# Kernel optimization log

Measured on AMD Instinct MI355X. Metric: run time of the kernel, lower is better.

Reference implementation:

```python
import jax, jax.numpy as jnp
import numpy as np

N_NODES = 100000
N_EDGES = 1600000
IN_DIM = 128
HID = 256
N_GRAPHS = 256
N_OUT = 2


def setup_inputs() -> dict:
    key = jax.random.key(0)
    ks = jax.random.split(key, 16)
    s_in = 1.0 / np.sqrt(IN_DIM)
    s_h = 1.0 / np.sqrt(HID)
    return {
        "x": jax.random.normal(ks[0], (N_NODES, IN_DIM), jnp.float32),
        "W_pool": jax.random.normal(ks[1], (IN_DIM, IN_DIM), jnp.float32) * s_in,
        "b_pool": jnp.zeros((IN_DIM,), jnp.float32),
        "W_self": jax.random.normal(ks[2], (IN_DIM, HID), jnp.float32) * s_in,
        "W_neigh": jax.random.normal(ks[3], (IN_DIM, HID), jnp.float32) * s_in,
        "b_sage": jnp.zeros((HID,), jnp.float32),
        "W1": jax.random.normal(ks[4], (HID, HID), jnp.float32) * s_h,
        "b1": jnp.zeros((HID,), jnp.float32),
        "W2": jax.random.normal(ks[5], (HID, HID), jnp.float32) * s_h,
        "b2": jnp.zeros((HID,), jnp.float32),
        "Wr": jax.random.normal(ks[6], (HID, N_OUT), jnp.float32) * s_h,
        "br": jnp.zeros((N_OUT,), jnp.float32),
        "src": jax.random.randint(ks[7], (N_EDGES,), 0, N_NODES, jnp.int32),
        "dst": jax.random.randint(ks[8], (N_EDGES,), 0, N_NODES, jnp.int32),
        "graph_id": jnp.sort(jax.random.randint(ks[9], (N_NODES,), 0, N_GRAPHS, jnp.int32)),
    }


def reference(x, W_pool, b_pool, W_self, W_neigh, b_sage, W1, b1, W2, b2, Wr, br, src, dst, graph_id):
    n = x.shape[0]
    # --- SAGEConv 'pool' aggregator ---
    m = jax.nn.relu(x @ W_pool + b_pool)                      # [N, IN]
    neigh = jax.ops.segment_max(m[src], dst, num_segments=n)  # max over in-neighbors
    neigh = jnp.where(jnp.isfinite(neigh), neigh, 0.0)        # isolated nodes -> 0 (DGL zero-init)
    h = jax.nn.relu(x @ W_self + neigh @ W_neigh + b_sage)    # [N, HID]
    # --- MLP stack ---
    h = jax.nn.relu(h @ W1 + b1)
    h = jax.nn.relu(h @ W2 + b2)
    # --- softmax_nodes: per-graph softmax over nodes, per feature ---
    gmax = jax.ops.segment_max(h, graph_id, num_segments=N_GRAPHS)
    gmax = jnp.where(jnp.isfinite(gmax), gmax, 0.0)
    z = jnp.exp(h - gmax[graph_id])                           # [N, HID]
    zsum = jax.ops.segment_sum(z, graph_id, num_segments=N_GRAPHS)
    hg = z / zsum[graph_id]
    # --- max_nodes readout ---
    final = jax.ops.segment_max(hg, graph_id, num_segments=N_GRAPHS)
    final = jnp.where(jnp.isfinite(final), final, 0.0)        # [G, HID]
    return final @ Wr + br                                    # [G, N_OUT]
```

## Files before the change

### kernel.cpp

```cpp
#include <hip/hip_runtime.h>

#define N_NODES  100000
#define N_EDGES  1600000
#define IN_DIM   128
#define HID      256
#define N_GRAPHS 256
#define ESHIFT   20.0f
#define BSH      7
#define NB2      782

typedef _Float16 f16x8 __attribute__((ext_vector_type(8)));
typedef float f32x16 __attribute__((ext_vector_type(16)));
#define MFMA16(a, b, c) __builtin_amdgcn_mfma_f32_32x32x16_f16((a), (b), (c), 0, 0, 0)

#define PKMAX(a, b) asm("v_pk_max_f16 %0, %0, %1" : "+v"(a) : "v"(b))

static __device__ __forceinline__ unsigned short f2h_bits(float f) {
    _Float16 h = (_Float16)f;
    return __builtin_bit_cast(unsigned short, h);
}
static __device__ __forceinline__ float h2f(unsigned short b) {
    return (float)__builtin_bit_cast(_Float16, b);
}

static __device__ __forceinline__ void decode_blk(int M, int& m0, int& n0)
{
    const int gmb = (M + 127) >> 7;
    const int l = blockIdx.x;
    int mb, nb;
    if ((int)gridDim.x == gmb) {
        mb = l; nb = 0;
    } else {
        const int nfull = (gmb >> 3) << 4;
        if (l < nfull) {
            mb = ((l >> 4) << 3) | (l & 7);
            nb = (l >> 3) & 1;
        } else {
            const int t = l - nfull, tm = gmb & 7;
            mb = (gmb & ~7) + (t % tm);
            nb = t / tm;
        }
    }
    m0 = mb * 128;
    n0 = nb * 128;
}

__global__ __launch_bounds__(256) void x_to_h(
    const float* __restrict__ in, unsigned short* __restrict__ xh, int n)
{
    int i = (blockIdx.x * 256 + threadIdx.x) * 4;
    if (i < n) {
        float4 v = *(const float4*)&in[i];
        ushort4 h;
        h.x = f2h_bits(v.x); h.y = f2h_bits(v.y);
        h.z = f2h_bits(v.z); h.w = f2h_bits(v.w);
        *(ushort4*)&xh[i] = h;
    }
}

__global__ __launch_bounds__(256) void w_split_h(
    const float* __restrict__ Wa, const float* __restrict__ Wb, int K1,
    int K, int N, unsigned short* __restrict__ hi, unsigned short* __restrict__ lo)
{
    int idx = blockIdx.x * 256 + threadIdx.x;
    if (idx >= K * N) return;
    int k = idx / N, n = idx - k * N;
    float w = (k < K1) ? Wa[(size_t)k * N + n] : Wb[(size_t)(k - K1) * N + n];
    unsigned short h = f2h_bits(w);
    unsigned short l = f2h_bits(w - h2f(h));
    hi[(size_t)n * K + k] = h;
    lo[(size_t)n * K + k] = l;
}

__global__ __launch_bounds__(256) void gemm_mfma_h(
    const unsigned short* __restrict__ A1, const unsigned short* __restrict__ A2,
    int K1, int Ktot,
    const unsigned short* __restrict__ Wh, const unsigned short* __restrict__ Wl,
    const float* __restrict__ bias, void* __restrict__ Cv,
    int M, int N, int mode)
{
    __shared__ __align__(16) short tA [128][32];
    __shared__ __align__(16) short tBh[128][32];
    __shared__ __align__(16) short tBl[128][32];

    const int tid  = threadIdx.x;
    int m0, n0;
    decode_blk(M, m0, n0);
    const int wave = tid >> 6, lane = tid & 63;
    const int mw   = (wave & 1) * 64, nw = (wave >> 1) * 64;
    const int lm   = lane & 31;

    const int rsub = lane >> 2;
    const int kqe  = ((lane & 3) ^ ((lane >> 3) & 3)) << 3;
    const int rw   = wave << 5;

    const int s4  = (lm >> 1) & 3;
    const int cB  = lane >> 5;
    const int ch0 = ((cB ^ s4) << 3);
    const int ch1 = (((2 | cB) ^ s4) << 3);
    const f16x8* a00 = (const f16x8*)&tA [mw + lm     ][ch0];
    const f16x8* a01 = (const f16x8*)&tA [mw + lm     ][ch1];
    const f16x8* a10 = (const f16x8*)&tA [mw + 32 + lm][ch0];
    const f16x8* a11 = (const f16x8*)&tA [mw + 32 + lm][ch1];
    const f16x8* bh00 = (const f16x8*)&tBh[nw + lm     ][ch0];
    const f16x8* bh01 = (const f16x8*)&tBh[nw + lm     ][ch1];
    const f16x8* bh10 = (const f16x8*)&tBh[nw + 32 + lm][ch0];
    const f16x8* bh11 = (const f16x8*)&tBh[nw + 32 + lm][ch1];
    const f16x8* bl00 = (const f16x8*)&tBl[nw + lm     ][ch0];
    const f16x8* bl01 = (const f16x8*)&tBl[nw + lm     ][ch1];
    const f16x8* bl10 = (const f16x8*)&tBl[nw + 32 + lm][ch0];
    const f16x8* bl11 = (const f16x8*)&tBl[nw + 32 + lm][ch1];

    f32x16 acc[4];
#pragma unroll
    for (int t = 0; t < 4; ++t)
#pragma unroll
        for (int i = 0; i < 16; ++i) acc[t][i] = 0.f;

    for (int kc = 0; kc < Ktot; kc += 32) {
        const unsigned short* Ab; int Astr, kl;
        if (kc < K1) { Ab = A1; Astr = K1;        kl = kc; }
        else         { Ab = A2; Astr = Ktot - K1; kl = kc - K1; }

        __syncthreads();
#pragma unroll
        for (int j = 0; j < 2; ++j) {
            const int tr = rw + j * 16;
            int row = m0 + tr + rsub; if (row >= M) row = M - 1;
            __builtin_amdgcn_global_load_lds(
                Ab + (size_t)row * Astr + kl + kqe, &tA[tr][0], 16, 0, 0);
            const size_t o = (size_t)(n0 + tr + rsub) * Ktot + kc + kqe;
            __builtin_amdgcn_global_load_lds(Wh + o, &tBh[tr][0], 16, 0, 0);
            __builtin_amdgcn_global_load_lds(Wl + o, &tBl[tr][0], 16, 0, 0);
        }
        __syncthreads();

        {
            f16x8 A0 = *a00, A1f = *a10;
            f16x8 B0h = *bh00, B1h = *bh10, B0l = *bl00, B1l = *bl10;
            acc[0] = MFMA16(A0,  B0h, acc[0]);
            acc[1] = MFMA16(A0,  B1h, acc[1]);
            acc[2] = MFMA16(A1f, B0h, acc[2]);
            acc[3] = MFMA16(A1f, B1h, acc[3]);
            acc[0] = MFMA16(A0,  B0l, acc[0]);
            acc[1] = MFMA16(A0,  B1l, acc[1]);
            acc[2] = MFMA16(A1f, B0l, acc[2]);
            acc[3] = MFMA16(A1f, B1l, acc[3]);
        }
        {
            f16x8 A0 = *a01, A1f = *a11;
            f16x8 B0h = *bh01, B1h = *bh11, B0l = *bl01, B1l = *bl11;
            acc[0] = MFMA16(A0,  B0h, acc[0]);
            acc[1] = MFMA16(A0,  B1h, acc[1]);
            acc[2] = MFMA16(A1f, B0h, acc[2]);
            acc[3] = MFMA16(A1f, B1h, acc[3]);
            acc[0] = MFMA16(A0,  B0l, acc[0]);
            acc[1] = MFMA16(A0,  B1l, acc[1]);
            acc[2] = MFMA16(A1f, B0l, acc[2]);
            acc[3] = MFMA16(A1f, B1l, acc[3]);
        }
    }

    const int rb = 4 * (lane >> 5);
#pragma unroll
    for (int ti = 0; ti < 2; ++ti)
#pragma unroll
    for (int tj = 0; tj < 2; ++tj) {
        f32x16 a = acc[ti * 2 + tj];
        int coln = n0 + nw + tj * 32 + lm;
        float bv = bias[coln];
#pragma unroll
        for (int reg = 0; reg < 16; ++reg) {
            int rrow = m0 + mw + ti * 32 + (reg & 3) + 8 * (reg >> 2) + rb;
            if (rrow < M) {
                float v = a[reg] + bv;
                v = v > 0.f ? v : 0.f;
                size_t o = (size_t)rrow * N + coln;
                if (mode == 0) ((float*)Cv)[o] = v;
                else           ((unsigned short*)Cv)[o] = f2h_bits(v);
            }
        }
    }
}

__global__ __launch_bounds__(256) void gemm_fused_sm(
    const unsigned short* __restrict__ A1,
    int Ktot,
    const unsigned short* __restrict__ Wh, const unsigned short* __restrict__ Wl,
    const float* __restrict__ bias, const int* __restrict__ gid,
    float* __restrict__ pm, float* __restrict__ ps,
    int M, int N)
{
    __shared__ __align__(16) short tA [128][32];
    __shared__ __align__(16) short tBh[128][32];
    __shared__ __align__(16) short tBl[128][32];

    const int tid  = threadIdx.x;
    int m0, n0;
    decode_blk(M, m0, n0);
    const int wave = tid >> 6, lane = tid & 63;
    const int mw   = (wave & 1) * 64, nw = (wave >> 1) * 64;
    const int lm   = lane & 31;

    const int rsub = lane >> 2;
    const int kqe  = ((lane & 3) ^ ((lane >> 3) & 3)) << 3;
    const int rw   = wave << 5;

    const int s4  = (lm >> 1) & 3;
    const int cB  = lane >> 5;
    const int ch0 = ((cB ^ s4) << 3);
    const int ch1 = (((2 | cB) ^ s4) << 3);
    const f16x8* a00 = (const f16x8*)&tA [mw + lm     ][ch0];
    const f16x8* a01 = (const f16x8*)&tA [mw + lm     ][ch1];
    const f16x8* a10 = (const f16x8*)&tA [mw + 32 + lm][ch0];
    const f16x8* a11 = (const f16x8*)&tA [mw + 32 + lm][ch1];
    const f16x8* bh00 = (const f16x8*)&tBh[nw + lm     ][ch0];
    const f16x8* bh01 = (const f16x8*)&tBh[nw + lm     ][ch1];
    const f16x8* bh10 = (const f16x8*)&tBh[nw + 32 + lm][ch0];
    const f16x8* bh11 = (const f16x8*)&tBh[nw + 32 + lm][ch1];
    const f16x8* bl00 = (const f16x8*)&tBl[nw + lm     ][ch0];
    const f16x8* bl01 = (const f16x8*)&tBl[nw + lm     ][ch1];
    const f16x8* bl10 = (const f16x8*)&tBl[nw + 32 + lm][ch0];
    const f16x8* bl11 = (const f16x8*)&tBl[nw + 32 + lm][ch1];

    f32x16 acc[4];
#pragma unroll
    for (int t = 0; t < 4; ++t)
#pragma unroll
        for (int i = 0; i < 16; ++i) acc[t][i] = 0.f;

    for (int kc = 0; kc < Ktot; kc += 32) {
        __syncthreads();
#pragma unroll
        for (int j = 0; j < 2; ++j) {
            const int tr = rw + j * 16;
            int row = m0 + tr + rsub; if (row >= M) row = M - 1;
            __builtin_amdgcn_global_load_lds(
                A1 + (size_t)row * Ktot + kc + kqe, &tA[tr][0], 16, 0, 0);
            const size_t o = (size_t)(n0 + tr + rsub) * Ktot + kc + kqe;
            __builtin_amdgcn_global_load_lds(Wh + o, &tBh[tr][0], 16, 0, 0);
            __builtin_amdgcn_global_load_lds(Wl + o, &tBl[tr][0], 16, 0, 0);
        }
        __syncthreads();

        {
            f16x8 A0 = *a00, A1f = *a10;
            f16x8 B0h = *bh00, B1h = *bh10, B0l = *bl00, B1l = *bl10;
            acc[0] = MFMA16(A0,  B0h, acc[0]);
            acc[1] = MFMA16(A0,  B1h, acc[1]);
            acc[2] = MFMA16(A1f, B0h, acc[2]);
            acc[3] = MFMA16(A1f, B1h, acc[3]);
            acc[0] = MFMA16(A0,  B0l, acc[0]);
            acc[1] = MFMA16(A0,  B1l, acc[1]);
            acc[2] = MFMA16(A1f, B0l, acc[2]);
            acc[3] = MFMA16(A1f, B1l, acc[3]);
        }
        {
            f16x8 A0 = *a01, A1f = *a11;
            f16x8 B0h = *bh01, B1h = *bh11, B0l = *bl01, B1l = *bl11;
            acc[0] = MFMA16(A0,  B0h, acc[0]);
            acc[1] = MFMA16(A0,  B1h, acc[1]);
            acc[2] = MFMA16(A1f, B0h, acc[2]);
            acc[3] = MFMA16(A1f, B1h, acc[3]);
            acc[0] = MFMA16(A0,  B0l, acc[0]);
            acc[1] = MFMA16(A0,  B1l, acc[1]);
            acc[2] = MFMA16(A1f, B0l, acc[2]);
            acc[3] = MFMA16(A1f, B1l, acc[3]);
        }
    }

    __syncthreads();
    float* sS = (float*)&tA[0][0];
    int*   sM = (int*)&tBh[0][0];
    for (int i = tid; i < 512; i += 256) { sS[i] = 0.f; sM[i] = 0; }
    __syncthreads();

    const int gfirst = gid[m0];
    const int rlast  = (m0 + 127 < M) ? (m0 + 127) : (M - 1);
    const int span   = gid[rlast] - gfirst + 1;

    const int rb = 4 * (lane >> 5);
#pragma unroll
    for (int tj = 0; tj < 2; ++tj) {
        int coln = n0 + nw + tj * 32 + lm;
        int cl   = coln - n0;
        float bv = bias[coln];
        int run_g = -1; float run_s = 0.f, run_m = 0.f;
#pragma unroll
        for (int ti = 0; ti < 2; ++ti) {
            f32x16 a = acc[ti * 2 + tj];
#pragma unroll
            for (int reg = 0; reg < 16; ++reg) {
                int rrow = m0 + mw + ti * 32 + (reg & 3) + 8 * (reg >> 2) + rb;
                if (rrow >= M) continue;
                float v = a[reg] + bv;
                v = v > 0.f ? v : 0.f;
                int g = gid[rrow];
                if (g != run_g) {
                    if (run_g >= 0) {
                        int slot = run_g - gfirst;
                        if (slot < 4) {
                            atomicAdd(&sS[slot * 128 + cl], run_s);
                            atomicMax(&sM[slot * 128 + cl], __float_as_int(run_m));
                        } else {
                            atomicAdd(&ps[(size_t)run_g * HID + coln], run_s);
                            atomicMax((int*)&pm[(size_t)run_g * HID + coln],
                                      __float_as_int(run_m));
                        }
                    }
                    run_g = g; run_s = 0.f; run_m = 0.f;
                }
                run_s += __expf(v - ESHIFT);
                run_m = fmaxf(run_m, v);
            }
        }
        if (run_g >= 0) {
            int slot = run_g - gfirst;
            if (slot < 4) {
                atomicAdd(&sS[slot * 128 + cl], run_s);
                atomicMax(&sM[slot * 128 + cl], __float_as_int(run_m));
            } else {
                atomicAdd(&ps[(size_t)run_g * HID + coln], run_s);
                atomicMax((int*)&pm[(size_t)run_g * HID + coln],
                          __float_as_int(run_m));
            }
        }
    }
    __syncthreads();

    int lim = (span < 4 ? span : 4) * 128;
    for (int i = tid; i < lim; i += 256) {
        int s = i >> 7, c = i & 127;
        float vs = sS[i];
        if (vs > 0.f) {
            int g = gfirst + s;
            atomicAdd(&ps[(size_t)g * HID + n0 + c], vs);
            atomicMax((int*)&pm[(size_t)g * HID + n0 + c], sM[i]);
        }
    }
}

__global__ __launch_bounds__(256) void part_count(
    const int* __restrict__ dst, int* __restrict__ btot, int E)
{
    __shared__ int sh[NB2];
    const int t = threadIdx.x;
    for (int i = t; i < NB2; i += 256) sh[i] = 0;
    __syncthreads();
    int base = blockIdx.x * 4096 + t;
#pragma unroll
    for (int i = 0; i < 16; ++i) {
        int e = base + i * 256;
        if (e < E) atomicAdd(&sh[dst[e] >> BSH], 1);
    }
    __syncthreads();
    for (int i = t; i < NB2; i += 256)
        if (sh[i]) atomicAdd(&btot[i], sh[i]);
}

__global__ __launch_bounds__(256) void scan_b(
    const int* __restrict__ btot, int* __restrict__ bstart,
    int* __restrict__ cursor, int total)
{
    __shared__ int sh[256];
    const int t = threadIdx.x;
    int a[4];
    int s = 0;
#pragma unroll
    for (int i = 0; i < 4; ++i) {
        int idx = t * 4 + i;
        a[i] = (idx < NB2) ? btot[idx] : 0;
        s += a[i];
    }
    sh[t] = s;
    __syncthreads();
    for (int off = 1; off < 256; off <<= 1) {
        int v = (t >= off) ? sh[t - off] : 0;
        __syncthreads();
        if (t >= off) sh[t] += v;
        __syncthreads();
    }
    int run = (t > 0) ? sh[t - 1] : 0;
#pragma unroll
    for (int i = 0; i < 4; ++i) {
        int idx = t * 4 + i;
        if (idx < NB2) { bstart[idx] = run; cursor[idx] = run; }
        run += a[i];
    }
    if (t == 0) bstart[NB2] = total;
}

__global__ __launch_bounds__(256) void part_scatter(
    const int* __restrict__ src, const int* __restrict__ dst,
    int* __restrict__ cursor, int2* __restrict__ pairs, int E)
{
    __shared__ int cnt[NB2], goff[NB2], fill[NB2];
    const int t = threadIdx.x;
    const int base = blockIdx.x * 4096;
    for (int i = t; i < NB2; i += 256) { cnt[i] = 0; fill[i] = 0; }
    __syncthreads();
    int myd[16];
#pragma unroll
    for (int i = 0; i < 16; ++i) {
        int e = base + t + i * 256;
        myd[i] = (e < E) ? dst[e] : -1;
        if (myd[i] >= 0) atomicAdd(&cnt[myd[i] >> BSH], 1);
    }
    __syncthreads();
    for (int i = t; i < NB2; i += 256)
        goff[i] = cnt[i] ? atomicAdd(&cursor[i], cnt[i]) : 0;
    __syncthreads();
#pragma unroll
    for (int i = 0; i < 16; ++i) {
        int e = base + t + i * 256;
        if (myd[i] >= 0) {
            int b = myd[i] >> BSH;
            int r = atomicAdd(&fill[b], 1);
            pairs[goff[b] + r] = make_int2(myd[i], src[e]);
        }
    }
}

__global__ __launch_bounds__(256) void bucket_sort(
    const int2* __restrict__ pairs, const int* __restrict__ bstart,
    int* __restrict__ csr_src, int* __restrict__ offs, int Nn, int E)
{
    __shared__ int cnt[128], off[128];
    const int b = blockIdx.x;
    const int t = threadIdx.x;
    const int lo = bstart[b], hi = bstart[b + 1];
    if (t < 128) cnt[t] = 0;
    __syncthreads();
    for (int e = lo + t; e < hi; e += 256)
        atomicAdd(&cnt[pairs[e].x & 127], 1);
    __syncthreads();
    if (t == 0) {
        int s = 0;
        for (int i = 0; i < 128; ++i) { off[i] = s; s += cnt[i]; }
    }
    __syncthreads();
    if (t < 128) {
        int node = (b << BSH) + t;
        if (node < Nn) offs[node] = lo + off[t];
        cnt[t] = off[t];
    }
    if (b == NB2 - 1 && t == 0) offs[Nn] = E;
    __syncthreads();
    for (int e = lo + t; e < hi; e += 256) {
        int2 p = pairs[e];
        int r = atomicAdd(&cnt[p.x & 127], 1);
        csr_src[lo + r] = p.y;
    }
}

__global__ __launch_bounds__(256) void csr_max_agg_h(
    const unsigned short* __restrict__ m, const int* __restrict__ csr_src,
    const int* __restrict__ offs, unsigned short* __restrict__ neigh, int Nn)
{
    const int node = (blockIdx.x * 256 + threadIdx.x) >> 6;
    const int lane = threadIdx.x & 63;
    if (node >= Nn) return;
    const int e0  = offs[node];
    const int end = offs[node + 1];
    const char* mc = (const char*)m;

    uint4 acc = make_uint4(0u, 0u, 0u, 0u);
    if (end > e0) {
        const unsigned fo = (unsigned)(lane & 15) << 4;
        const int sub = lane >> 4;
        for (int base = e0; base < end; base += 64) {
            int ee = base + lane;
            int sl = csr_src[ee < end ? ee : (end - 1)];
            int cnt = end - base; if (cnt > 64) cnt = 64;
            int iters = (cnt + 3) >> 2;
            for (int j = 0; j < iters; ++j) {
                int s = __shfl(sl, (j << 2) | sub);
                uint4 v = *(const uint4*)(mc + (((unsigned)s << 8) | fo));
                PKMAX(acc.x, v.x);
                PKMAX(acc.y, v.y);
                PKMAX(acc.z, v.z);
                PKMAX(acc.w, v.w);
            }
        }
        uint4 o;
        o.x = __shfl_xor(acc.x, 16); o.y = __shfl_xor(acc.y, 16);
        o.z = __shfl_xor(acc.z, 16); o.w = __shfl_xor(acc.w, 16);
        PKMAX(acc.x, o.x); PKMAX(acc.y, o.y);
        PKMAX(acc.z, o.z); PKMAX(acc.w, o.w);
        o.x = __shfl_xor(acc.x, 32); o.y = __shfl_xor(acc.y, 32);
        o.z = __shfl_xor(acc.z, 32); o.w = __shfl_xor(acc.w, 32);
        PKMAX(acc.x, o.x); PKMAX(acc.y, o.y);
        PKMAX(acc.z, o.z); PKMAX(acc.w, o.w);
    }
    if (lane < 16)
        *(uint4*)((char*)neigh + (((size_t)node << 8) | ((unsigned)lane << 4))) = acc;
}

__global__ __launch_bounds__(256) void softmax_merge(
    const float* __restrict__ pm, const float* __restrict__ ps,
    const float* __restrict__ Wr, const float* __restrict__ brv,
    float* __restrict__ out)
{
    const int g = blockIdx.x;
    const int j = threadIdx.x;

    float M = pm[(size_t)g * HID + j];
    float S = ps[(size_t)g * HID + j];
    float fm = (S > 0.f) ? __expf(M - ESHIFT) / S : 0.f;

    float p0 = fm * Wr[j * 2 + 0];
    float p1 = fm * Wr[j * 2 + 1];
#pragma unroll
    for (int off = 32; off > 0; off >>= 1) {
        p0 += __shfl_down(p0, off);
        p1 += __shfl_down(p1, off);
    }
    __shared__ float red[8];
    int wv = j >> 6, ln = j & 63;
    if (ln == 0) { red[wv * 2] = p0; red[wv * 2 + 1] = p1; }
    __syncthreads();
    if (j == 0) out[g * 2 + 0] = red[0] + red[2] + red[4] + red[6] + brv[0];
    if (j == 1) out[g * 2 + 1] = red[1] + red[3] + red[5] + red[7] + brv[1];
}

extern "C" void kernel_launch(void* const* d_in, const int* in_sizes, int n_in,
                              void* d_out, int out_size, void* d_ws, size_t ws_size,
                              hipStream_t stream)
{
    const float* x      = (const float*)d_in[0];
    const float* W_pool = (const float*)d_in[1];
    const float* b_pool = (const float*)d_in[2];
    const float* W_self = (const float*)d_in[3];
    const float* W_neigh= (const float*)d_in[4];
    const float* b_sage = (const float*)d_in[5];
    const float* W1     = (const float*)d_in[6];
    const float* b1     = (const float*)d_in[7];
    const float* W2     = (const float*)d_in[8];
    const float* b2     = (const float*)d_in[9];
    const float* Wr     = (const float*)d_in[10];
    const float* br     = (const float*)d_in[11];
    const int*   src    = (const int*)d_in[12];
    const int*   dst    = (const int*)d_in[13];
    const int*   gid    = (const int*)d_in[14];

    const int Nn = N_NODES, E = N_EDGES;
    char* ws = (char*)d_ws;

    unsigned short* xh    = (unsigned short*)(ws + 0);
    unsigned short* m_buf = (unsigned short*)(ws + 25600000);
    unsigned short* neigh = (unsigned short*)(ws + 51200000);
    int2*           pairs = (int2*)(ws + 76800000);
    int*            btot  = (int*)(ws + 89600000);
    int*            bstart= btot + NB2;
    int*            cursor= bstart + NB2 + 1;
    float*          pm    = (float*)(ws + 90000000);
    float*          ps    = pm + (size_t)N_GRAPHS * HID;
    int*            offs  = (int*)(ws + 91000000);
    int*            csr_src = (int*)(ws + 91500000);
    unsigned short* h1    = (unsigned short*)(ws + 102400000);
    unsigned short* h2    = (unsigned short*)(ws + 153600000);

    char* srcws = (char*)(void*)src;
    unsigned short* wpool_h = (unsigned short*)(srcws + 0);
    unsigned short* wpool_l = wpool_h + 128 * 128;
    unsigned short* wsage_h = wpool_l + 128 * 128;
    unsigned short* wsage_l = wsage_h + 256 * 256;
    unsigned short* w1_h    = wsage_l + 256 * 256;
    unsigned short* w1_l    = w1_h + 256 * 256;
    unsigned short* w2_h    = w1_l + 256 * 256;
    unsigned short* w2_l    = w2_h + 256 * 256;

    dim3 blk(256);
    const int gm = (Nn + 127) / 128;
    const int pchunks = (E + 4095) / 4096;

    hipMemsetAsync(btot, 0, NB2 * sizeof(int), stream);
    hipMemsetAsync(pm, 0, (size_t)2 * N_GRAPHS * HID * sizeof(float), stream);

    x_to_h<<<dim3((Nn * IN_DIM / 4 + 255) / 256), blk, 0, stream>>>(
        x, xh, Nn * IN_DIM);

    part_count<<<dim3(pchunks), blk, 0, stream>>>(dst, btot, E);
    scan_b<<<dim3(1), blk, 0, stream>>>(btot, bstart, cursor, E);
    part_scatter<<<dim3(pchunks), blk, 0, stream>>>(src, dst, cursor, pairs, E);
    bucket_sort<<<dim3(NB2), blk, 0, stream>>>(pairs, bstart, csr_src, offs, Nn, E);

    w_split_h<<<dim3((128 * 128 + 255) / 256), blk, 0, stream>>>(
        W_pool, W_pool, 128, 128, 128, wpool_h, wpool_l);
    w_split_h<<<dim3((256 * 256 + 255) / 256), blk, 0, stream>>>(
        W_self, W_neigh, 128, 256, 256, wsage_h, wsage_l);
    w_split_h<<<dim3((256 * 256 + 255) / 256), blk, 0, stream>>>(
        W1, W1, 256, 256, 256, w1_h, w1_l);
    w_split_h<<<dim3((256 * 256 + 255) / 256), blk, 0, stream>>>(
        W2, W2, 256, 256, 256, w2_h, w2_l);

    gemm_mfma_h<<<dim3(gm), blk, 0, stream>>>(
        xh, xh, 128, 128, wpool_h, wpool_l, b_pool, m_buf, Nn, 128, 1);

    csr_max_agg_h<<<dim3((Nn * 64 + 255) / 256), blk, 0, stream>>>(
        m_buf, csr_src, offs, neigh, Nn);

    gemm_mfma_h<<<dim3(2 * gm), blk, 0, stream>>>(
        xh, neigh, 128, 256, wsage_h, wsage_l, b_sage, h1, Nn, 256, 1);

    gemm_mfma_h<<<dim3(2 * gm), blk, 0, stream>>>(
        h1, h1, 256, 256, w1_h, w1_l, b1, h2, Nn, 256, 1);

    gemm_fused_sm<<<dim3(2 * gm), blk, 0, stream>>>(
        h2, 256, w2_h, w2_l, b2, gid, pm, ps, Nn, 256);

    softmax_merge<<<dim3(N_GRAPHS), blk, 0, stream>>>(pm, ps, Wr, br, (float*)d_out);
}
```

Measured before the change: 471.1 us.

## Use persistent GEMMs with register-resident weights and double-buffered A tiles

Replaces the three 256-wide GEMMs with persistent 512-thread kernels on a 256-block grid. Each wave keeps its 32 output columns of the split-fp16 weights in registers, and 64-row A tiles stream through a double-buffered LDS pipeline controlled by manual vmcnt waits. This removes the repeated weight tile loads and per-K-step block barriers of the old tiled kernel. The softmax-stat epilogue now keeps a running per-graph accumulator across a block's whole contiguous row range, with 8 shared slots. The costs are very high register pressure, which may limit occupancy, and a fixed grid size that can leave some blocks with an extra tile.

Result: faster. 434.5 us (-7.8%).

```diff
diff --git a/kernel.cpp b/kernel.cpp
--- a/kernel.cpp
+++ b/kernel.cpp
@@ -14,6 +14,9 @@
 #define MFMA16(a, b, c) __builtin_amdgcn_mfma_f32_32x32x16_f16((a), (b), (c), 0, 0, 0)
 
 #define PKMAX(a, b) asm("v_pk_max_f16 %0, %0, %1" : "+v"(a) : "v"(b))
+
+#define BARX() __builtin_amdgcn_s_barrier()
+#define WAITVM(N) asm volatile("s_waitcnt vmcnt(" #N ")" ::: "memory")
 
 static __device__ __forceinline__ unsigned short f2h_bits(float f) {
     _Float16 h = (_Float16)f;
@@ -183,115 +186,170 @@
     }
 }
 
-__global__ __launch_bounds__(256) void gemm_fused_sm(
-    const unsigned short* __restrict__ A1,
-    int Ktot,
+static __device__ __forceinline__ void stage_tile64(
+    const unsigned short* __restrict__ A1, const unsigned short* __restrict__ A2,
+    int K1, int M, int r0g, short* bufb, int wave, int lane)
+{
+    const int l5 = lane >> 5;
+    const int s  = lane & 31;
+#pragma unroll
+    for (int i = 0; i < 4; ++i) {
+        const int p    = wave * 4 + i;
+        const int rloc = 2 * p + l5;
+        int row = r0g + rloc; if (row >= M) row = M - 1;
+        const int c8 = ((s ^ ((2 * i + l5) & 7)) << 3);
+        const unsigned short* sp = (c8 < K1)
+            ? A1 + (size_t)row * K1 + c8
+            : A2 + (size_t)row * (256 - K1) + (c8 - K1);
+        __builtin_amdgcn_global_load_lds(sp, bufb + p * 512, 16, 0, 0);
+    }
+}
+
+__global__ __launch_bounds__(512, 2) void gemm_bstat(
+    const unsigned short* __restrict__ A1, const unsigned short* __restrict__ A2,
+    int K1,
+    const unsigned short* __restrict__ Wh, const unsigned short* __restrict__ Wl,
+    const float* __restrict__ bias, unsigned short* __restrict__ C,
+    unsigned short* __restrict__ dummy, int M)
+{
+    __shared__ __align__(16) short buf[2][64][256];
+
+    const int tid = threadIdx.x, wave = tid >> 6, lane = tid & 63;
+    const int lm = lane & 31, hib = lane >> 5;
+    const int col = wave * 32 + lm;
+    const int hi8 = hib * 8;
+
+    f16x8 Bh[16], Bl[16];
+#pragma unroll
+    for (int k = 0; k < 16; ++k) {
+        const size_t o = (size_t)col * 256 + k * 16 + hi8;
+        Bh[k] = *(const f16x8*)(Wh + o);
+        Bl[k] = *(const f16x8*)(Wl + o);
+    }
+
+    const int nt = (M + 63) >> 6;
+    const int G = gridDim.x, b = blockIdx.x;
+    const int q = nt / G, r = nt % G;
+    const int t0  = b * q + (b < r ? b : r);
+    const int ntl = q + (b < r ? 1 : 0);
+
+    const int rq    = (lm >> 1) & 3;
+    const int abase = lm * 512 + ((hib ^ (lm & 1)) << 4);
+    const float bv  = bias[col];
+    const int rb    = 4 * hib;
+
+    stage_tile64(A1, A2, K1, M, t0 << 6, &buf[0][0][0], wave, lane);
+    if (ntl > 1)
+        stage_tile64(A1, A2, K1, M, (t0 + 1) << 6, &buf[1][0][0], wave, lane);
+
+    for (int t = 0; t < ntl; ++t) {
+        if (t == 0) { if (ntl > 1) WAITVM(4); else WAITVM(0); }
+        else if (t + 1 < ntl) WAITVM(36);
+        else WAITVM(32);
+        BARX();
+
+        f32x16 acc0, acc1;
+#pragma unroll
+        for (int i = 0; i < 16; ++i) { acc0[i] = 0.f; acc1[i] = 0.f; }
+        const char* lb = (const char*)&buf[t & 1][0][0];
+#pragma unroll
+        for (int k = 0; k < 16; ++k) {
+            const int koff = ((k ^ rq) << 5);
+            f16x8 a0 = *(const f16x8*)(lb + abase + koff);
+            f16x8 a1 = *(const f16x8*)(lb + abase + koff + 16384);
+            acc0 = MFMA16(a0, Bh[k], acc0);
+            acc1 = MFMA16(a1, Bh[k], acc1);
+            acc0 = MFMA16(a0, Bl[k], acc0);
+            acc1 = MFMA16(a1, Bl[k], acc1);
+        }
+        BARX();
+
+        const int r0g = (t0 + t) << 6;
+#pragma unroll
+        for (int reg = 0; reg < 16; ++reg) {
+            const int rr0 = r0g + (reg & 3) + 8 * (reg >> 2) + rb;
+            const int rr1 = rr0 + 32;
+            unsigned short* d0 = (rr0 < M) ? C + (size_t)rr0 * 256 + col : dummy + tid;
+            unsigned short* d1 = (rr1 < M) ? C + (size_t)rr1 * 256 + col : dummy + tid;
+            *d0 = f2h_bits(fmaxf(acc0[reg] + bv, 0.f));
+            *d1 = f2h_bits(fmaxf(acc1[reg] + bv, 0.f));
+        }
+        if (t + 2 < ntl)
+            stage_tile64(A1, A2, K1, M, (t0 + t + 2) << 6,
+                         &buf[t & 1][0][0], wave, lane);
+    }
+}
+
+__global__ __launch_bounds__(512, 2) void gemm_bstat_sm(
+    const unsigned short* __restrict__ A,
     const unsigned short* __restrict__ Wh, const unsigned short* __restrict__ Wl,
     const float* __restrict__ bias, const int* __restrict__ gid,
-    float* __restrict__ pm, float* __restrict__ ps,
-    int M, int N)
-{
-    __shared__ __align__(16) short tA [128][32];
-    __shared__ __align__(16) short tBh[128][32];
-    __shared__ __align__(16) short tBl[128][32];
-
-    const int tid  = threadIdx.x;
-    int m0, n0;
-    decode_blk(M, m0, n0);
-    const int wave = tid >> 6, lane = tid & 63;
-    const int mw   = (wave & 1) * 64, nw = (wave >> 1) * 64;
-    const int lm   = lane & 31;
-
-    const int rsub = lane >> 2;
-    const int kqe  = ((lane & 3) ^ ((lane >> 3) & 3)) << 3;
-    const int rw   = wave << 5;
-
-    const int s4  = (lm >> 1) & 3;
-    const int cB  = lane >> 5;
-    const int ch0 = ((cB ^ s4) << 3);
-    const int ch1 = (((2 | cB) ^ s4) << 3);
-    const f16x8* a00 = (const f16x8*)&tA [mw + lm     ][ch0];
-    const f16x8* a01 = (const f16x8*)&tA [mw + lm     ][ch1];
-    const f16x8* a10 = (const f16x8*)&tA [mw + 32 + lm][ch0];
-    const f16x8* a11 = (const f16x8*)&tA [mw + 32 + lm][ch1];
-    const f16x8* bh00 = (const f16x8*)&tBh[nw + lm     ][ch0];
-    const f16x8* bh01 = (const f16x8*)&tBh[nw + lm     ][ch1];
-    const f16x8* bh10 = (const f16x8*)&tBh[nw + 32 + lm][ch0];
-    const f16x8* bh11 = (const f16x8*)&tBh[nw + 32 + lm][ch1];
-    const f16x8* bl00 = (const f16x8*)&tBl[nw + lm     ][ch0];
-    const f16x8* bl01 = (const f16x8*)&tBl[nw + lm     ][ch1];
-    const f16x8* bl10 = (const f16x8*)&tBl[nw + 32 + lm][ch0];
-    const f16x8* bl11 = (const f16x8*)&tBl[nw + 32 + lm][ch1];
-
-    f32x16 acc[4];
-#pragma unroll
-    for (int t = 0; t < 4; ++t)
-#pragma unroll
-        for (int i = 0; i < 16; ++i) acc[t][i] = 0.f;
-
-    for (int kc = 0; kc < Ktot; kc += 32) {
-        __syncthreads();
-#pragma unroll
-        for (int j = 0; j < 2; ++j) {
-            const int tr = rw + j * 16;
-            int row = m0 + tr + rsub; if (row >= M) row = M - 1;
-            __builtin_amdgcn_global_load_lds(
-                A1 + (size_t)row * Ktot + kc + kqe, &tA[tr][0], 16, 0, 0);
-            const size_t o = (size_t)(n0 + tr + rsub) * Ktot + kc + kqe;
-            __builtin_amdgcn_global_load_lds(Wh + o, &tBh[tr][0], 16, 0, 0);
-            __builtin_amdgcn_global_load_lds(Wl + o, &tBl[tr][0], 16, 0, 0);
-        }
-        __syncthreads();
-
-        {
-            f16x8 A0 = *a00, A1f = *a10;
-            f16x8 B0h = *bh00, B1h = *bh10, B0l = *bl00, B1l = *bl10;
-            acc[0] = MFMA16(A0,  B0h, acc[0]);
-            acc[1] = MFMA16(A0,  B1h, acc[1]);
-            acc[2] = MFMA16(A1f, B0h, acc[2]);
-            acc[3] = MFMA16(A1f, B1h, acc[3]);
-            acc[0] = MFMA16(A0,  B0l, acc[0]);
-            acc[1] = MFMA16(A0,  B1l, acc[1]);
-            acc[2] = MFMA16(A1f, B0l, acc[2]);
-            acc[3] = MFMA16(A1f, B1l, acc[3]);
-        }
-        {
-            f16x8 A0 = *a01, A1f = *a11;
-            f16x8 B0h = *bh01, B1h = *bh11, B0l = *bl01, B1l = *bl11;
-            acc[0] = MFMA16(A0,  B0h, acc[0]);
-            acc[1] = MFMA16(A0,  B1h, acc[1]);
-            acc[2] = MFMA16(A1f, B0h, acc[2]);
-            acc[3] = MFMA16(A1f, B1h, acc[3]);
-            acc[0] = MFMA16(A0,  B0l, acc[0]);
-            acc[1] = MFMA16(A0,  B1l, acc[1]);
-            acc[2] = MFMA16(A1f, B0l, acc[2]);
-            acc[3] = MFMA16(A1f, B1l, acc[3]);
-        }
-    }
-
-    __syncthreads();
-    float* sS = (float*)&tA[0][0];
-    int*   sM = (int*)&tBh[0][0];
-    for (int i = tid; i < 512; i += 256) { sS[i] = 0.f; sM[i] = 0; }
-    __syncthreads();
-
-    const int gfirst = gid[m0];
-    const int rlast  = (m0 + 127 < M) ? (m0 + 127) : (M - 1);
-    const int span   = gid[rlast] - gfirst + 1;
-
-    const int rb = 4 * (lane >> 5);
-#pragma unroll
-    for (int tj = 0; tj < 2; ++tj) {
-        int coln = n0 + nw + tj * 32 + lm;
-        int cl   = coln - n0;
-        float bv = bias[coln];
-        int run_g = -1; float run_s = 0.f, run_m = 0.f;
-#pragma unroll
-        for (int ti = 0; ti < 2; ++ti) {
-            f32x16 a = acc[ti * 2 + tj];
+    float* __restrict__ pm, float* __restrict__ ps, int M)
+{
+    __shared__ __align__(16) short buf[2][64][256];
+    __shared__ float sS[8 * 256];
+    __shared__ int   sM[8 * 256];
+
+    const int tid = threadIdx.x, wave = tid >> 6, lane = tid & 63;
+    const int lm = lane & 31, hib = lane >> 5;
+    const int col = wave * 32 + lm;
+    const int hi8 = hib * 8;
+
+    for (int i = tid; i < 2048; i += 512) { sS[i] = 0.f; sM[i] = 0; }
+
+    f16x8 Bh[16], Bl[16];
+#pragma unroll
+    for (int k = 0; k < 16; ++k) {
+        const size_t o = (size_t)col * 256 + k * 16 + hi8;
+        Bh[k] = *(const f16x8*)(Wh + o);
+        Bl[k] = *(const f16x8*)(Wl + o);
+    }
+
+    const int nt = (M + 63) >> 6;
+    const int G = gridDim.x, b = blockIdx.x;
+    const int q = nt / G, r = nt % G;
+    const int t0  = b * q + (b < r ? b : r);
+    const int ntl = q + (b < r ? 1 : 0);
+
+    const int rq    = (lm >> 1) & 3;
+    const int abase = lm * 512 + ((hib ^ (lm & 1)) << 4);
+    const float bv  = bias[col];
+    const int rb    = 4 * hib;
+    const int gfirst = gid[t0 << 6];
+
+    stage_tile64(A, A, 256, M, t0 << 6, &buf[0][0][0], wave, lane);
+    if (ntl > 1)
+        stage_tile64(A, A, 256, M, (t0 + 1) << 6, &buf[1][0][0], wave, lane);
+
+    int run_g = -1; float run_s = 0.f, run_m = 0.f;
+
+    for (int t = 0; t < ntl; ++t) {
+        if (t + 1 < ntl) WAITVM(4); else WAITVM(0);
+        BARX();
+
+        f32x16 acc0, acc1;
+#pragma unroll
+        for (int i = 0; i < 16; ++i) { acc0[i] = 0.f; acc1[i] = 0.f; }
+        const char* lb = (const char*)&buf[t & 1][0][0];
+#pragma unroll
+        for (int k = 0; k < 16; ++k) {
+            const int koff = ((k ^ rq) << 5);
+            f16x8 a0 = *(const f16x8*)(lb + abase + koff);
+            f16x8 a1 = *(const f16x8*)(lb + abase + koff + 16384);
+            acc0 = MFMA16(a0, Bh[k], acc0);
+            acc1 = MFMA16(a1, Bh[k], acc1);
+            acc0 = MFMA16(a0, Bl[k], acc0);
+            acc1 = MFMA16(a1, Bl[k], acc1);
+        }
+        BARX();
+
+        const int r0g = (t0 + t) << 6;
+#pragma unroll
+        for (int sub = 0; sub < 2; ++sub) {
+            const f32x16& a = sub ? acc1 : acc0;
 #pragma unroll
             for (int reg = 0; reg < 16; ++reg) {
-                int rrow = m0 + mw + ti * 32 + (reg & 3) + 8 * (reg >> 2) + rb;
+                const int rrow = r0g + sub * 32 + (reg & 3) + 8 * (reg >> 2) + rb;
                 if (rrow >= M) continue;
                 float v = a[reg] + bv;
                 v = v > 0.f ? v : 0.f;
@@ -299,12 +357,12 @@
                 if (g != run_g) {
                     if (run_g >= 0) {
                         int slot = run_g - gfirst;
-                        if (slot < 4) {
-                            atomicAdd(&sS[slot * 128 + cl], run_s);
-                            atomicMax(&sM[slot * 128 + cl], __float_as_int(run_m));
+                        if (slot < 8) {
+                            atomicAdd(&sS[slot * 256 + col], run_s);
+                            atomicMax(&sM[slot * 256 + col], __float_as_int(run_m));
                         } else {
-                            atomicAdd(&ps[(size_t)run_g * HID + coln], run_s);
-                            atomicMax((int*)&pm[(size_t)run_g * HID + coln],
+                            atomicAdd(&ps[(size_t)run_g * HID + col], run_s);
+                            atomicMax((int*)&pm[(size_t)run_g * HID + col],
                                       __float_as_int(run_m));
                         }
                     }
@@ -314,28 +372,31 @@
                 run_m = fmaxf(run_m, v);
             }
         }
-        if (run_g >= 0) {
-            int slot = run_g - gfirst;
-            if (slot < 4) {
-                atomicAdd(&sS[slot * 128 + cl], run_s);
-                atomicMax(&sM[slot * 128 + cl], __float_as_int(run_m));
-            } else {
-                atomicAdd(&ps[(size_t)run_g * HID + coln], run_s);
-                atomicMax((int*)&pm[(size_t)run_g * HID + coln],
-                          __float_as_int(run_m));
-            }
-        }
-    }
-    __syncthreads();
-
-    int lim = (span < 4 ? span : 4) * 128;
-    for (int i = tid; i < lim; i += 256) {
-        int s = i >> 7, c = i & 127;
+        if (t + 2 < ntl)
+            stage_tile64(A, A, 256, M, (t0 + t + 2) << 6,
+                         &buf[t & 1][0][0], wave, lane);
+    }
+
+    if (run_g >= 0) {
+        int slot = run_g - gfirst;
+        if (slot < 8) {
+            atomicAdd(&sS[slot * 256 + col], run_s);
+            atomicMax(&sM[slot * 256 + col], __float_as_int(run_m));
+        } else {
+            atomicAdd(&ps[(size_t)run_g * HID + col], run_s);
+            atomicMax((int*)&pm[(size_t)run_g * HID + col], __float_as_int(run_m));
+        }
+    }
+    __syncthreads();
+
+    int lastrow = ((t0 + ntl) << 6) - 1; if (lastrow >= M) lastrow = M - 1;
+    int span = gid[lastrow] - gfirst + 1; if (span > 8) span = 8;
+    for (int i = tid; i < span * 256; i += 512) {
         float vs = sS[i];
         if (vs > 0.f) {
-            int g = gfirst + s;
-            atomicAdd(&ps[(size_t)g * HID + n0 + c], vs);
-            atomicMax((int*)&pm[(size_t)g * HID + n0 + c], sM[i]);
+            int g = gfirst + (i >> 8), c = i & 255;
+            atomicAdd(&ps[(size_t)g * HID + c], vs);
+            atomicMax((int*)&pm[(size_t)g * HID + c], sM[i]);
         }
     }
 }
@@ -559,6 +620,7 @@
     int*            csr_src = (int*)(ws + 91500000);
     unsigned short* h1    = (unsigned short*)(ws + 102400000);
     unsigned short* h2    = (unsigned short*)(ws + 153600000);
+    unsigned short* dummy = (unsigned short*)pairs;
 
     char* srcws = (char*)(void*)src;
     unsigned short* wpool_h = (unsigned short*)(srcws + 0);
@@ -600,14 +662,14 @@
     csr_max_agg_h<<<dim3((Nn * 64 + 255) / 256), blk, 0, stream>>>(
         m_buf, csr_src, offs, neigh, Nn);
 
-    gemm_mfma_h<<<dim3(2 * gm), blk, 0, stream>>>(
-        xh, neigh, 128, 256, wsage_h, wsage_l, b_sage, h1, Nn, 256, 1);
-
-    gemm_mfma_h<<<dim3(2 * gm), blk, 0, stream>>>(
-        h1, h1, 256, 256, w1_h, w1_l, b1, h2, Nn, 256, 1);
-
-    gemm_fused_sm<<<dim3(2 * gm), blk, 0, stream>>>(
-        h2, 256, w2_h, w2_l, b2, gid, pm, ps, Nn, 256);
+    gemm_bstat<<<dim3(256), dim3(512), 0, stream>>>(
+        xh, neigh, 128, wsage_h, wsage_l, b_sage, h1, dummy, Nn);
+
+    gemm_bstat<<<dim3(256), dim3(512), 0, stream>>>(
+        h1, h1, 256, w1_h, w1_l, b1, h2, dummy, Nn);
+
+    gemm_bstat_sm<<<dim3(256), dim3(512), 0, stream>>>(
+        h2, w2_h, w2_l, b2, gid, pm, ps, Nn);
 
     softmax_merge<<<dim3(N_GRAPHS), blk, 0, stream>>>(pm, ps, Wr, br, (float*)d_out);
 }
```
